# Optimization experiments

Hardware: AMD Instinct MI355X
Metric: run time of the kernel (lower is better)

## Reference

```python
import jax, jax.numpy as jnp
import numpy as np

LAYERS, UNITS, B, T = 3, 1024, 128, 256


def setup_inputs() -> dict:
    key = jax.random.key(0)
    k1, k2, k3, k4, k5 = jax.random.split(key, 5)
    scale = 0.03  # keep gate pre-activations in a sane range
    return {
        "input_seq": jax.random.normal(k1, (B, T, UNITS), dtype=jnp.float32),
        "initial_states": jax.random.normal(k2, (B, UNITS, LAYERS), dtype=jnp.float32),
        "W": jax.random.normal(k3, (LAYERS, UNITS, 3 * UNITS), dtype=jnp.float32) * scale,
        "U": jax.random.normal(k4, (LAYERS, UNITS, 3 * UNITS), dtype=jnp.float32) * scale,
        "b": jax.random.normal(k5, (LAYERS, 2, 3 * UNITS), dtype=jnp.float32) * scale,
    }


def _gru_layer(x, h0, Wl, Ul, bl):
    """Keras GRU (reset_after=True), inference mode. x: [B,T,F], h0: [B,U]."""
    u = h0.shape[-1]
    # Precompute input projections for all timesteps: [B,T,3U] -> scan over T.
    xw = jnp.einsum("btf,fg->btg", x, Wl) + bl[0]
    xw_t = jnp.swapaxes(xw, 0, 1)  # [T,B,3U]

    def step(h, xw_step):
        hu = h @ Ul + bl[1]  # [B,3U]
        xz, xr, xh = xw_step[:, :u], xw_step[:, u:2 * u], xw_step[:, 2 * u:]
        hz, hr, hh = hu[:, :u], hu[:, u:2 * u], hu[:, 2 * u:]
        z = jax.nn.sigmoid(xz + hz)
        r = jax.nn.sigmoid(xr + hr)
        hhat = jnp.tanh(xh + r * hh)
        h_new = z * h + (1.0 - z) * hhat
        return h_new, h_new

    h_last, ys = jax.lax.scan(step, h0, xw_t)
    return jnp.swapaxes(ys, 0, 1), h_last  # [B,T,U], [B,U]


def reference(input_seq, initial_states, W, U, b):
    x = input_seq
    states = []
    for i in range(LAYERS):
        x, h = _gru_layer(x, initial_states[:, :, i], W[i], U[i], b[i])
        states.append(h)
    return x, jnp.stack(states, axis=-1)  # [B,T,U], [B,U,L]
```

## Files before the change

kernel.cpp:

```cpp
#include <hip/hip_runtime.h>
#include <cstdint>
#include <cstddef>


#define UNITS 1024
#define U3 3072
#define BATCH 128
#define TSTEPS 256

typedef _Float16 h16;
typedef __attribute__((ext_vector_type(8))) _Float16 h16x8;
typedef __attribute__((ext_vector_type(4))) _Float16 h16x4;
typedef __attribute__((ext_vector_type(4))) float f32x4;
typedef __attribute__((ext_vector_type(4))) unsigned int u32x4;

#define GAS __attribute__((address_space(1)))
#define LAS __attribute__((address_space(3)))
#define ASYNC16(g, l) __builtin_amdgcn_global_load_lds((const GAS unsigned int*)(g), (LAS unsigned int*)(l), 16, 0, 0)

__device__ __forceinline__ float sigmf(float x) { return 1.0f / (1.0f + __expf(-x)); }
__device__ __forceinline__ float tanhf_fast(float x) { return 2.0f / (1.0f + __expf(-2.0f * x)) - 1.0f; }

__global__ void k_cvt_x(const float* __restrict__ x, h16* __restrict__ xo) {
  const int m = blockIdx.x;
  const int t = m >> 7, b = m & 127;
  const int u = threadIdx.x << 2;
  const float4 v = *(const float4*)(x + (size_t)((b << 8) + t) * UNITS + u);
  h16x4 o; o[0] = (h16)v.x; o[1] = (h16)v.y; o[2] = (h16)v.z; o[3] = (h16)v.w;
  *(h16x4*)(xo + (size_t)m * UNITS + u) = o;
}

__global__ void k_trans(const float* __restrict__ src, h16* __restrict__ dst) {
  __shared__ float sT[32][33];
  const int l = blockIdx.z;
  const int n0 = blockIdx.x << 5, k0 = blockIdx.y << 5;
  const int tx = threadIdx.x, ty = threadIdx.y;
  const float* s = src + (size_t)l * UNITS * U3;
  h16* d = dst + (size_t)l * U3 * UNITS;
#pragma unroll
  for (int r = 0; r < 4; ++r)
    sT[ty + r * 8][tx] = s[(size_t)(k0 + ty + r * 8) * U3 + n0 + tx];
  __syncthreads();
#pragma unroll
  for (int r = 0; r < 4; ++r)
    d[(size_t)(n0 + ty + r * 8) * UNITS + k0 + tx] = (h16)sT[tx][ty + r * 8];
}

__global__ void k_cvt_h(const float* __restrict__ init, h16* __restrict__ h0) {
  const int idx = blockIdx.x * 256 + threadIdx.x;
  const int l = idx >> 17, r = idx & 131071;
  h0[idx] = (h16)init[(size_t)r * 3 + l];
}

__global__ void k_zero(int* __restrict__ p, int n) {
  const int i = blockIdx.x * 256 + threadIdx.x;
  if (i < n) p[i] = 0;
}

__global__ __launch_bounds__(256) void k_gemm_xw(
    const h16* __restrict__ A, const h16* __restrict__ Bt,
    const float* __restrict__ bias, h16* __restrict__ C) {
  __shared__ __align__(16) h16 sA[128 * 32];
  __shared__ __align__(16) h16 sB[128 * 32];
  const int tid = threadIdx.x;
  const int lane = tid & 63, wave = tid >> 6;
  const int wm = (wave & 1) << 6, wn = (wave >> 1) << 6;
  const int m0 = blockIdx.x << 7;
  const int n0 = blockIdx.y << 7;
  const int crow = tid >> 2, ck = (tid & 3) << 3;
  const int fm = lane & 15, fq = lane >> 4;
  f32x4 acc[4][4] = {};
  for (int k0 = 0; k0 < 1024; k0 += 32) {
    ASYNC16(A + (size_t)(m0 + crow) * 1024 + k0 + ck,      sA + wave * 512);
    ASYNC16(A + (size_t)(m0 + 64 + crow) * 1024 + k0 + ck, sA + 2048 + wave * 512);
    ASYNC16(Bt + (size_t)(n0 + crow) * 1024 + k0 + ck,      sB + wave * 512);
    ASYNC16(Bt + (size_t)(n0 + 64 + crow) * 1024 + k0 + ck, sB + 2048 + wave * 512);
    __syncthreads();
    h16x8 af[4], bfv[4];
#pragma unroll
    for (int i = 0; i < 4; ++i)
      af[i] = *(const h16x8*)(sA + (wm + i * 16 + fm) * 32 + fq * 8);
#pragma unroll
    for (int j = 0; j < 4; ++j)
      bfv[j] = *(const h16x8*)(sB + (wn + j * 16 + fm) * 32 + fq * 8);
#pragma unroll
    for (int i = 0; i < 4; ++i)
#pragma unroll
      for (int j = 0; j < 4; ++j)
        acc[i][j] = __builtin_amdgcn_mfma_f32_16x16x32_f16(af[i], bfv[j], acc[i][j], 0, 0, 0);
    __syncthreads();
  }
#pragma unroll
  for (int j = 0; j < 4; ++j) {
    const int col = n0 + wn + j * 16 + fm;
    const float bv = bias[col];
#pragma unroll
    for (int i = 0; i < 4; ++i) {
      const int row = m0 + wm + i * 16 + fq * 4;
#pragma unroll
      for (int r = 0; r < 4; ++r)
        C[(size_t)(row + r) * U3 + col] = (h16)(acc[i][j][r] + bv);
    }
  }
}

__global__ __launch_bounds__(128, 1) void k_rec(
    const h16* __restrict__ Ut,
    const float* __restrict__ b1,
    const h16* __restrict__ xw,
    const h16* __restrict__ h0l,
    h16* __restrict__ P0,
    h16* __restrict__ P1,
    h16* __restrict__ y16,
    float* __restrict__ yf,
    float* __restrict__ st,
    int* __restrict__ cnt,
    const int tgt) {
  __shared__ __align__(16) h16 sU[49152];
  const int tid = threadIdx.x;
  const int lane = tid & 63, w = tid >> 6;
  const int b = blockIdx.x;
  const int c = b & 63, rg = b >> 6;
  const int c0 = c << 4;
  const int fm = lane & 15, fq = lane >> 4;

#pragma unroll
  for (int kk = 0; kk < 32; ++kk) {
#pragma unroll
    for (int g = 0; g < 3; ++g) {
      const int i = kk * 3 + g;
      if ((i & 1) == w)
        ASYNC16(Ut + (size_t)((g << 10) + c0 + fm) * 1024 + (kk << 5) + (fq << 3),
                sU + (size_t)i * 512);
    }
  }
  const int col = c0 + fm;
  const float bz = b1[col], br = b1[1024 + col], bh = b1[2048 + col];
  const int r0 = (rg << 5) + (w << 4);
  const int rowA = r0 + fm;
  const int rQ = r0 + (fq << 2);
  int* cbase = cnt + (rg << 8);
  __syncthreads();

  h16x8 Bz[16], Br[16], Bh[16];
#pragma unroll
  for (int kk = 0; kk < 16; ++kk) {
    const h16* bb = sU + (size_t)(kk * 3) * 512 + (lane << 3);
    Bz[kk] = *(const h16x8*)(bb);
    Br[kk] = *(const h16x8*)(bb + 512);
    Bh[kk] = *(const h16x8*)(bb + 1024);
  }

  for (int t = 0; t < TSTEPS; ++t) {
    if (t > 0) {
      const int* cp = cbase + t - 1;
      int f;
      do {
        asm volatile("global_load_dword %0, %1, off sc0 sc1\n\ts_waitcnt vmcnt(0)"
                     : "=v"(f) : "v"(cp) : "memory");
      } while (f < tgt);
    }
    const h16* hin = (t == 0) ? h0l : ((t & 1) ? P0 : P1);
    h16* hout = (t & 1) ? P1 : P0;

    u32x4 raw[32];
    const h16* Ab = hin + (size_t)rowA * 1024 + (fq << 3);
#pragma unroll
    for (int kk = 0; kk < 32; ++kk)
      asm volatile("global_load_dwordx4 %0, %1, off offset:%2 sc0 sc1"
                   : "=v"(raw[kk]) : "v"(Ab), "n"(kk * 64));
    unsigned int hpu[4];
    const h16* hqa = hin + (size_t)rQ * 1024 + col;
    const h16* hqb = hqa + 2048;
    asm volatile("global_load_ushort %0, %1, off sc0 sc1"             : "=v"(hpu[0]) : "v"(hqa));
    asm volatile("global_load_ushort %0, %1, off offset:2048 sc0 sc1" : "=v"(hpu[1]) : "v"(hqa));
    asm volatile("global_load_ushort %0, %1, off sc0 sc1"             : "=v"(hpu[2]) : "v"(hqb));
    asm volatile("global_load_ushort %0, %1, off offset:2048 sc0 sc1" : "=v"(hpu[3]) : "v"(hqb));
    unsigned int xwb[12];
    {
      const h16* xq = xw + (size_t)(t * 128 + rQ) * U3 + col;
#pragma unroll
      for (int r = 0; r < 4; ++r) {
        const h16* xa = xq + (size_t)r * U3;
        const h16* xb2 = xa + 2048;
        asm volatile("global_load_ushort %0, %1, off"             : "=v"(xwb[r * 3 + 0]) : "v"(xa));
        asm volatile("global_load_ushort %0, %1, off offset:2048" : "=v"(xwb[r * 3 + 1]) : "v"(xa));
        asm volatile("global_load_ushort %0, %1, off"             : "=v"(xwb[r * 3 + 2]) : "v"(xb2));
      }
    }

    f32x4 a0 = {}, a1 = {}, a2 = {};
#pragma unroll
    for (int ch = 0; ch < 4; ++ch) {
      if (ch == 0) asm volatile("s_waitcnt vmcnt(40)" ::: "memory");
      if (ch == 1) asm volatile("s_waitcnt vmcnt(32)" ::: "memory");
      if (ch == 2) asm volatile("s_waitcnt vmcnt(24)" ::: "memory");
      if (ch == 3) asm volatile("s_waitcnt vmcnt(16)" ::: "memory");
      __builtin_amdgcn_sched_barrier(0);
#pragma unroll
      for (int kk = ch * 8; kk < ch * 8 + 8; ++kk) {
        union { u32x4 u; h16x8 h; } ac; ac.u = raw[kk];
        if (kk < 16) {
          a0 = __builtin_amdgcn_mfma_f32_16x16x32_f16(ac.h, Bz[kk], a0, 0, 0, 0);
          a1 = __builtin_amdgcn_mfma_f32_16x16x32_f16(ac.h, Br[kk], a1, 0, 0, 0);
          a2 = __builtin_amdgcn_mfma_f32_16x16x32_f16(ac.h, Bh[kk], a2, 0, 0, 0);
        } else {
          const h16* bb = sU + (size_t)(kk * 3) * 512 + (lane << 3);
          const h16x8 vz = *(const h16x8*)(bb);
          const h16x8 vr = *(const h16x8*)(bb + 512);
          const h16x8 vh = *(const h16x8*)(bb + 1024);
          a0 = __builtin_amdgcn_mfma_f32_16x16x32_f16(ac.h, vz, a0, 0, 0, 0);
          a1 = __builtin_amdgcn_mfma_f32_16x16x32_f16(ac.h, vr, a1, 0, 0, 0);
          a2 = __builtin_amdgcn_mfma_f32_16x16x32_f16(ac.h, vh, a2, 0, 0, 0);
        }
      }
    }
    asm volatile("s_waitcnt vmcnt(0)" ::: "memory");
    __builtin_amdgcn_sched_barrier(0);

    h16* so = hout + (size_t)rQ * 1024 + col;
    float hn[4];
#pragma unroll
    for (int r = 0; r < 4; ++r) {
      union { unsigned short s; h16 h; } cv;
      cv.s = (unsigned short)hpu[r];         const float hp = (float)cv.h;
      cv.s = (unsigned short)xwb[r * 3 + 0]; const float xz = (float)cv.h;
      cv.s = (unsigned short)xwb[r * 3 + 1]; const float xr = (float)cv.h;
      cv.s = (unsigned short)xwb[r * 3 + 2]; const float xh = (float)cv.h;
      const float z   = sigmf(xz + a0[r] + bz);
      const float rgt = sigmf(xr + a1[r] + br);
      const float hh  = tanhf_fast(xh + rgt * (a2[r] + bh));
      hn[r] = z * hp + (1.0f - z) * hh;
      union { unsigned short s; h16 h; } ov; ov.h = (h16)hn[r];
      const unsigned int ob = ov.s;
      if (r == 0) asm volatile("global_store_short %0, %1, off sc0 sc1"             :: "v"(so), "v"(ob) : "memory");
      if (r == 1) asm volatile("global_store_short %0, %1, off offset:2048 sc0 sc1" :: "v"(so), "v"(ob) : "memory");
      if (r == 2) asm volatile("global_store_short %0, %1, off sc0 sc1"             :: "v"(so + 2048), "v"(ob) : "memory");
      if (r == 3) asm volatile("global_store_short %0, %1, off offset:2048 sc0 sc1" :: "v"(so + 2048), "v"(ob) : "memory");
    }
    asm volatile("s_waitcnt vmcnt(0)" ::: "memory");
    if (lane == 0)
      (void)__hip_atomic_fetch_add(cbase + t, 1, __ATOMIC_RELAXED,
                                   __HIP_MEMORY_SCOPE_AGENT);
#pragma unroll
    for (int r = 0; r < 4; ++r) {
      const int row = rQ + r;
      if (y16) y16[(size_t)(t * 128 + row) * 1024 + col] = (h16)hn[r];
      if (yf)  yf[(size_t)(row * 256 + t) * 1024 + col] = hn[r];
      if (t == 255) st[(size_t)(row * 1024 + col) * 3] = hn[r];
    }
  }
}

extern "C" void kernel_launch(void* const* d_in, const int* in_sizes, int n_in,
                              void* d_out, int out_size, void* d_ws, size_t ws_size,
                              hipStream_t stream) {
  const float* x_in  = (const float*)d_in[0];
  const float* h0_in = (const float*)d_in[1];
  const float* W     = (const float*)d_in[2];
  const float* U     = (const float*)d_in[3];
  const float* bias  = (const float*)d_in[4];
  float* out = (float*)d_out;

  char* ws = (char*)d_ws;
  h16* x16 = (h16*)(ws);
  h16* xw  = (h16*)(ws + 67108864);
  h16* Wt  = (h16*)(ws + 268435456);
  h16* Ut  = (h16*)(ws + 287309824);
  h16* h0b = (h16*)(ws + 306184192);
  h16* P0  = (h16*)(ws + 306970624);

  h16* P1A   = (h16*)((char*)d_out + 134217728 - 262144);
  int* cntA  = (int*)((char*)d_out + 134217728 - 262144 - 16384);
  h16* P1B   = (h16*)ws;
  int* cntB  = (int*)(ws + 262144);

  k_cvt_x<<<TSTEPS * BATCH, 256, 0, stream>>>(x_in, x16);
  k_trans<<<dim3(96, 32, 3), dim3(32, 8), 0, stream>>>(W, Wt);
  k_trans<<<dim3(96, 32, 3), dim3(32, 8), 0, stream>>>(U, Ut);
  k_cvt_h<<<1536, 256, 0, stream>>>(h0_in, h0b);
  k_zero<<<4, 256, 0, stream>>>(cntA, 1024);

  for (int l = 0; l < 3; ++l) {
    const float* b0 = bias + (size_t)l * 6144;
    const float* b1 = bias + (size_t)l * 6144 + 3072;
    k_gemm_xw<<<dim3(256, 24), 256, 0, stream>>>(x16, Wt + (size_t)l * U3 * UNITS, b0, xw);
    if (l == 2) k_zero<<<4, 256, 0, stream>>>(cntB, 1024);
    h16* P1   = (l < 2) ? P1A : P1B;
    int* cnt  = (l < 2) ? cntA : cntB;
    const int tgt = (l < 2) ? (l + 1) * 128 : 128;
    h16* y16p  = (l < 2) ? x16 : nullptr;
    float* yfp = (l == 2) ? out : nullptr;
    float* stp = out + 33554432 + l;
    k_rec<<<256, 128, 0, stream>>>(Ut + (size_t)l * U3 * UNITS, b1, xw,
                                   h0b + (size_t)l * BATCH * UNITS,
                                   P0, P1, y16p, yfp, stp, cnt, tgt);
  }
}
```

Before: 6.064 ms.

## Write hidden state directly into sequence history buffer and prefetch next-step xw

The recurrent kernel stops ping-ponging the hidden state through two scratch buffers plus a separate y16 copy. Each step's h is written straight into the x16 history buffer at slot s and read back from slot s-1, so one set of stores serves as both recurrence state and next-layer input. The xw gate inputs for step s+1 are loaded after the elementwise update, overlapping their latency with the flag wait. Cache-bypass bits are relaxed (sc0 dropped), and the register-resident U half is replaced by LDS reads every step. The costs are extra LDS traffic per step and weaker coherence bits that rely on the acquire fence and sc1 for cross-block visibility.

```diff
diff --git a/kernel.cpp b/kernel.cpp
--- a/kernel.cpp
+++ b/kernel.cpp
@@ -109,14 +109,13 @@
     const float* __restrict__ b1,
     const h16* __restrict__ xw,
     const h16* __restrict__ h0l,
-    h16* __restrict__ P0,
-    h16* __restrict__ P1,
-    h16* __restrict__ y16,
+    h16* __restrict__ hist,
     float* __restrict__ yf,
     float* __restrict__ st,
     int* __restrict__ cnt,
     const int tgt) {
   __shared__ __align__(16) h16 sU[49152];
+  __builtin_amdgcn_fence(__ATOMIC_ACQUIRE, "agent");
   const int tid = threadIdx.x;
   const int lane = tid & 63, w = tid >> 6;
   const int b = blockIdx.x;
@@ -140,45 +139,93 @@
   const int rowA = r0 + fm;
   const int rQ = r0 + (fq << 2);
   int* cbase = cnt + (rg << 8);
+
+  unsigned int xwb[12];
+  {
+    const h16* xq = xw + (size_t)rQ * U3 + col;
+#pragma unroll
+    for (int r = 0; r < 4; ++r) {
+      const h16* xa = xq + (size_t)r * U3;
+      const h16* xb2 = xa + 2048;
+      asm volatile("global_load_ushort %0, %1, off"             : "=v"(xwb[r * 3 + 0]) : "v"(xa));
+      asm volatile("global_load_ushort %0, %1, off offset:2048" : "=v"(xwb[r * 3 + 1]) : "v"(xa));
+      asm volatile("global_load_ushort %0, %1, off"             : "=v"(xwb[r * 3 + 2]) : "v"(xb2));
+    }
+  }
   __syncthreads();
 
-  h16x8 Bz[16], Br[16], Bh[16];
-#pragma unroll
-  for (int kk = 0; kk < 16; ++kk) {
-    const h16* bb = sU + (size_t)(kk * 3) * 512 + (lane << 3);
-    Bz[kk] = *(const h16x8*)(bb);
-    Br[kk] = *(const h16x8*)(bb + 512);
-    Bh[kk] = *(const h16x8*)(bb + 1024);
-  }
-
-  for (int t = 0; t < TSTEPS; ++t) {
-    if (t > 0) {
-      const int* cp = cbase + t - 1;
+  for (int s = 0; s < TSTEPS; ++s) {
+    if (s > 0) {
+      const int* cp = cbase + s - 1;
       int f;
       do {
-        asm volatile("global_load_dword %0, %1, off sc0 sc1\n\ts_waitcnt vmcnt(0)"
+        asm volatile("global_load_dword %0, %1, off sc1\n\ts_waitcnt vmcnt(0)"
                      : "=v"(f) : "v"(cp) : "memory");
       } while (f < tgt);
     }
-    const h16* hin = (t == 0) ? h0l : ((t & 1) ? P0 : P1);
-    h16* hout = (t & 1) ? P1 : P0;
+    const h16* hin = (s == 0) ? h0l : hist + (size_t)(s - 1) * 131072;
 
     u32x4 raw[32];
     const h16* Ab = hin + (size_t)rowA * 1024 + (fq << 3);
 #pragma unroll
     for (int kk = 0; kk < 32; ++kk)
-      asm volatile("global_load_dwordx4 %0, %1, off offset:%2 sc0 sc1"
+      asm volatile("global_load_dwordx4 %0, %1, off offset:%2"
                    : "=v"(raw[kk]) : "v"(Ab), "n"(kk * 64));
     unsigned int hpu[4];
     const h16* hqa = hin + (size_t)rQ * 1024 + col;
     const h16* hqb = hqa + 2048;
-    asm volatile("global_load_ushort %0, %1, off sc0 sc1"             : "=v"(hpu[0]) : "v"(hqa));
-    asm volatile("global_load_ushort %0, %1, off offset:2048 sc0 sc1" : "=v"(hpu[1]) : "v"(hqa));
-    asm volatile("global_load_ushort %0, %1, off sc0 sc1"             : "=v"(hpu[2]) : "v"(hqb));
-    asm volatile("global_load_ushort %0, %1, off offset:2048 sc0 sc1" : "=v"(hpu[3]) : "v"(hqb));
-    unsigned int xwb[12];
+    asm volatile("global_load_ushort %0, %1, off"             : "=v"(hpu[0]) : "v"(hqa));
+    asm volatile("global_load_ushort %0, %1, off offset:2048" : "=v"(hpu[1]) : "v"(hqa));
+    asm volatile("global_load_ushort %0, %1, off"             : "=v"(hpu[2]) : "v"(hqb));
+    asm volatile("global_load_ushort %0, %1, off offset:2048" : "=v"(hpu[3]) : "v"(hqb));
+
+    f32x4 a0 = {}, a1 = {}, a2 = {};
+#pragma unroll
+    for (int ch = 0; ch < 4; ++ch) {
+      if (ch == 0) asm volatile("s_waitcnt vmcnt(28)" ::: "memory");
+      if (ch == 1) asm volatile("s_waitcnt vmcnt(20)" ::: "memory");
+      if (ch == 2) asm volatile("s_waitcnt vmcnt(12)" ::: "memory");
+      if (ch == 3) asm volatile("s_waitcnt vmcnt(4)"  ::: "memory");
+      __builtin_amdgcn_sched_barrier(0);
+#pragma unroll
+      for (int kk = ch * 8; kk < ch * 8 + 8; ++kk) {
+        union { u32x4 u; h16x8 h; } ac; ac.u = raw[kk];
+        const h16* bb = sU + (size_t)(kk * 3) * 512 + (lane << 3);
+        const h16x8 vz = *(const h16x8*)(bb);
+        const h16x8 vr = *(const h16x8*)(bb + 512);
+        const h16x8 vh = *(const h16x8*)(bb + 1024);
+        a0 = __builtin_amdgcn_mfma_f32_16x16x32_f16(ac.h, vz, a0, 0, 0, 0);
+        a1 = __builtin_amdgcn_mfma_f32_16x16x32_f16(ac.h, vr, a1, 0, 0, 0);
+        a2 = __builtin_amdgcn_mfma_f32_16x16x32_f16(ac.h, vh, a2, 0, 0, 0);
+      }
+    }
+    asm volatile("s_waitcnt vmcnt(0)" ::: "memory");
+    __builtin_amdgcn_sched_barrier(0);
+
+    h16* so = hist + (size_t)s * 131072 + (size_t)rQ * 1024 + col;
+    float hn[4];
+#pragma unroll
+    for (int r = 0; r < 4; ++r) {
+      union { unsigned short u; h16 h; } cv;
+      cv.u = (unsigned short)hpu[r];         const float hp = (float)cv.h;
+      cv.u = (unsigned short)xwb[r * 3 + 0]; const float xz = (float)cv.h;
+      cv.u = (unsigned short)xwb[r * 3 + 1]; const float xr = (float)cv.h;
+      cv.u = (unsigned short)xwb[r * 3 + 2]; const float xh = (float)cv.h;
+      const float z   = sigmf(xz + a0[r] + bz);
+      const float rgt = sigmf(xr + a1[r] + br);
+      const float hh  = tanhf_fast(xh + rgt * (a2[r] + bh));
+      hn[r] = z * hp + (1.0f - z) * hh;
+      union { unsigned short u; h16 h; } ov; ov.h = (h16)hn[r];
+      const unsigned int ob = ov.u;
+      if (r == 0) asm volatile("global_store_short %0, %1, off sc1"             :: "v"(so), "v"(ob) : "memory");
+      if (r == 1) asm volatile("global_store_short %0, %1, off offset:2048 sc1" :: "v"(so), "v"(ob) : "memory");
+      if (r == 2) asm volatile("global_store_short %0, %1, off sc1"             :: "v"(so + 2048), "v"(ob) : "memory");
+      if (r == 3) asm volatile("global_store_short %0, %1, off offset:2048 sc1" :: "v"(so + 2048), "v"(ob) : "memory");
+    }
+
     {
-      const h16* xq = xw + (size_t)(t * 128 + rQ) * U3 + col;
+      const int sn = (s + 1) & 255;
+      const h16* xq = xw + (size_t)(sn * 128 + rQ) * U3 + col;
 #pragma unroll
       for (int r = 0; r < 4; ++r) {
         const h16* xa = xq + (size_t)r * U3;
@@ -188,66 +235,19 @@
         asm volatile("global_load_ushort %0, %1, off"             : "=v"(xwb[r * 3 + 2]) : "v"(xb2));
       }
     }
-
-    f32x4 a0 = {}, a1 = {}, a2 = {};
-#pragma unroll
-    for (int ch = 0; ch < 4; ++ch) {
-      if (ch == 0) asm volatile("s_waitcnt vmcnt(40)" ::: "memory");
-      if (ch == 1) asm volatile("s_waitcnt vmcnt(32)" ::: "memory");
-      if (ch == 2) asm volatile("s_waitcnt vmcnt(24)" ::: "memory");
-      if (ch == 3) asm volatile("s_waitcnt vmcnt(16)" ::: "memory");
-      __builtin_amdgcn_sched_barrier(0);
-#pragma unroll
-      for (int kk = ch * 8; kk < ch * 8 + 8; ++kk) {
-        union { u32x4 u; h16x8 h; } ac; ac.u = raw[kk];
-        if (kk < 16) {
-          a0 = __builtin_amdgcn_mfma_f32_16x16x32_f16(ac.h, Bz[kk], a0, 0, 0, 0);
-          a1 = __builtin_amdgcn_mfma_f32_16x16x32_f16(ac.h, Br[kk], a1, 0, 0, 0);
-          a2 = __builtin_amdgcn_mfma_f32_16x16x32_f16(ac.h, Bh[kk], a2, 0, 0, 0);
-        } else {
-          const h16* bb = sU + (size_t)(kk * 3) * 512 + (lane << 3);
-          const h16x8 vz = *(const h16x8*)(bb);
-          const h16x8 vr = *(const h16x8*)(bb + 512);
-          const h16x8 vh = *(const h16x8*)(bb + 1024);
-          a0 = __builtin_amdgcn_mfma_f32_16x16x32_f16(ac.h, vz, a0, 0, 0, 0);
-          a1 = __builtin_amdgcn_mfma_f32_16x16x32_f16(ac.h, vr, a1, 0, 0, 0);
-          a2 = __builtin_amdgcn_mfma_f32_16x16x32_f16(ac.h, vh, a2, 0, 0, 0);
-        }
-      }
-    }
-    asm volatile("s_waitcnt vmcnt(0)" ::: "memory");
-    __builtin_amdgcn_sched_barrier(0);
-
-    h16* so = hout + (size_t)rQ * 1024 + col;
-    float hn[4];
-#pragma unroll
-    for (int r = 0; r < 4; ++r) {
-      union { unsigned short s; h16 h; } cv;
-      cv.s = (unsigned short)hpu[r];         const float hp = (float)cv.h;
-      cv.s = (unsigned short)xwb[r * 3 + 0]; const float xz = (float)cv.h;
-      cv.s = (unsigned short)xwb[r * 3 + 1]; const float xr = (float)cv.h;
-      cv.s = (unsigned short)xwb[r * 3 + 2]; const float xh = (float)cv.h;
-      const float z   = sigmf(xz + a0[r] + bz);
-      const float rgt = sigmf(xr + a1[r] + br);
-      const float hh  = tanhf_fast(xh + rgt * (a2[r] + bh));
-      hn[r] = z * hp + (1.0f - z) * hh;
-      union { unsigned short s; h16 h; } ov; ov.h = (h16)hn[r];
-      const unsigned int ob = ov.s;
-      if (r == 0) asm volatile("global_store_short %0, %1, off sc0 sc1"             :: "v"(so), "v"(ob) : "memory");
-      if (r == 1) asm volatile("global_store_short %0, %1, off offset:2048 sc0 sc1" :: "v"(so), "v"(ob) : "memory");
-      if (r == 2) asm volatile("global_store_short %0, %1, off sc0 sc1"             :: "v"(so + 2048), "v"(ob) : "memory");
-      if (r == 3) asm volatile("global_store_short %0, %1, off offset:2048 sc0 sc1" :: "v"(so + 2048), "v"(ob) : "memory");
-    }
-    asm volatile("s_waitcnt vmcnt(0)" ::: "memory");
+    asm volatile("s_waitcnt vmcnt(12)" ::: "memory");
     if (lane == 0)
-      (void)__hip_atomic_fetch_add(cbase + t, 1, __ATOMIC_RELAXED,
+      (void)__hip_atomic_fetch_add(cbase + s, 1, __ATOMIC_RELAXED,
                                    __HIP_MEMORY_SCOPE_AGENT);
-#pragma unroll
-    for (int r = 0; r < 4; ++r) {
-      const int row = rQ + r;
-      if (y16) y16[(size_t)(t * 128 + row) * 1024 + col] = (h16)hn[r];
-      if (yf)  yf[(size_t)(row * 256 + t) * 1024 + col] = hn[r];
-      if (t == 255) st[(size_t)(row * 1024 + col) * 3] = hn[r];
+    if (yf) {
+#pragma unroll
+      for (int r = 0; r < 4; ++r)
+        yf[(size_t)((rQ + r) * 256 + s) * 1024 + col] = hn[r];
+    }
+    if (s == 255) {
+#pragma unroll
+      for (int r = 0; r < 4; ++r)
+        st[(size_t)((rQ + r) * 1024 + col) * 3] = hn[r];
     }
   }
 }
@@ -268,32 +268,22 @@
   h16* Wt  = (h16*)(ws + 268435456);
   h16* Ut  = (h16*)(ws + 287309824);
   h16* h0b = (h16*)(ws + 306184192);
-  h16* P0  = (h16*)(ws + 306970624);
-
-  h16* P1A   = (h16*)((char*)d_out + 134217728 - 262144);
-  int* cntA  = (int*)((char*)d_out + 134217728 - 262144 - 16384);
-  h16* P1B   = (h16*)ws;
-  int* cntB  = (int*)(ws + 262144);
+  int* cnt = (int*)(ws + 306970624);
 
   k_cvt_x<<<TSTEPS * BATCH, 256, 0, stream>>>(x_in, x16);
   k_trans<<<dim3(96, 32, 3), dim3(32, 8), 0, stream>>>(W, Wt);
   k_trans<<<dim3(96, 32, 3), dim3(32, 8), 0, stream>>>(U, Ut);
   k_cvt_h<<<1536, 256, 0, stream>>>(h0_in, h0b);
-  k_zero<<<4, 256, 0, stream>>>(cntA, 1024);
+  k_zero<<<4, 256, 0, stream>>>(cnt, 1024);
 
   for (int l = 0; l < 3; ++l) {
     const float* b0 = bias + (size_t)l * 6144;
     const float* b1 = bias + (size_t)l * 6144 + 3072;
     k_gemm_xw<<<dim3(256, 24), 256, 0, stream>>>(x16, Wt + (size_t)l * U3 * UNITS, b0, xw);
-    if (l == 2) k_zero<<<4, 256, 0, stream>>>(cntB, 1024);
-    h16* P1   = (l < 2) ? P1A : P1B;
-    int* cnt  = (l < 2) ? cntA : cntB;
-    const int tgt = (l < 2) ? (l + 1) * 128 : 128;
-    h16* y16p  = (l < 2) ? x16 : nullptr;
     float* yfp = (l == 2) ? out : nullptr;
     float* stp = out + 33554432 + l;
     k_rec<<<256, 128, 0, stream>>>(Ut + (size_t)l * U3 * UNITS, b1, xw,
                                    h0b + (size_t)l * BATCH * UNITS,
-                                   P0, P1, y16p, yfp, stp, cnt, tgt);
-  }
-}
+                                   x16, yfp, stp, cnt, 128 * (l + 1));
+  }
+}
```

Result: no change. 5.993 ms (-1.2%).
